# Optimization experiments

Measured on AMD Instinct MI355X. Metric: run time of the kernel, lower is better.

Reference implementation:

```python
import jax, jax.numpy as jnp
import numpy as np

N_NODES = 50000
NNZ = 800000
HYPER_DIM = 128
N_LAYERS = 2
LEAKY = 0.2
LN_EPS = 1e-5


def setup_inputs() -> dict:
    key = jax.random.key(0)
    k1, k2, k3, k4 = jax.random.split(key, 4)
    return {
        "ego_embeddings": jax.random.normal(k1, (N_NODES, HYPER_DIM), dtype=jnp.float32),
        "adj_vals": jax.random.uniform(k2, (NNZ,), dtype=jnp.float32),
        "ln_gamma": jnp.ones((N_LAYERS, HYPER_DIM), dtype=jnp.float32),
        "ln_beta": jnp.zeros((N_LAYERS, HYPER_DIM), dtype=jnp.float32),
        "adj_rows": jax.random.randint(k3, (NNZ,), 0, N_NODES, dtype=jnp.int32),
        "adj_cols": jax.random.randint(k4, (NNZ,), 0, N_NODES, dtype=jnp.int32),
        "n_users": 25000,
    }


def _spmm(rows, cols, vals, x, n_out):
    # y = A @ x for sparse A in COO (rows, cols, vals): gather + segment-sum
    return jax.ops.segment_sum(vals[:, None] * x[cols], rows, num_segments=n_out)


def _layer_norm(x, gamma, beta):
    mu = jnp.mean(x, axis=-1, keepdims=True)
    var = jnp.mean(jnp.square(x - mu), axis=-1, keepdims=True)
    return (x - mu) * jax.lax.rsqrt(var + LN_EPS) * gamma + beta


def reference(ego_embeddings, adj_vals, ln_gamma, ln_beta, adj_rows, adj_cols, n_users):
    res = ego_embeddings
    embs = ego_embeddings
    for k in range(N_LAYERS):
        # adj.T @ embs  (rows of A^T are cols of A)
        ht = _spmm(adj_cols, adj_rows, adj_vals, embs, N_NODES)
        # adj @ (adj.T @ embs)
        h = _spmm(adj_rows, adj_cols, adj_vals, ht, N_NODES)
        if k != N_LAYERS - 1:
            h = jnp.where(h >= 0, h, LEAKY * h)  # LeakyReLU
        embs = _layer_norm(h, ln_gamma[k], ln_beta[k]) + res
    user_emb = embs[:n_users]
    item_emb = embs[n_users:]
    return (user_emb, item_emb)
```

## Files before the change

kernel.cpp:

```cpp
#include <hip/hip_runtime.h>
#include <hip/hip_bf16.h>

#define HD 128
#define PB 256
#define LEAKY 0.2f
#define LN_EPS 1e-5f

__device__ __forceinline__ unsigned short bfr(float f) {
    unsigned int b = __float_as_uint(f);
    return (unsigned short)((b + 0x7fffu + ((b >> 16) & 1u)) >> 16);
}
__device__ __forceinline__ float blo(unsigned int u) { return __uint_as_float(u << 16); }
__device__ __forceinline__ float bhi(unsigned int u) { return __uint_as_float(u & 0xffff0000u); }

__global__ __launch_bounds__(256) void f32_to_bf16(
    const float* __restrict__ x, unsigned short* __restrict__ y, int n4) {
    int i = blockIdx.x * 256 + threadIdx.x;
    if (i >= n4) return;
    float4 f = ((const float4*)x)[i];
    ushort4 u;
    u.x = bfr(f.x); u.y = bfr(f.y); u.z = bfr(f.z); u.w = bfr(f.w);
    ((ushort4*)y)[i] = u;
}


__global__ __launch_bounds__(256) void part_count(
    const int* __restrict__ rows, const int* __restrict__ cols,
    int* __restrict__ counts, int nnz) {
    __shared__ int cR[64], cC[64];
    if (threadIdx.x < 64) { cR[threadIdx.x] = 0; cC[threadIdx.x] = 0; }
    __syncthreads();
    int chunk = (nnz + PB - 1) / PB;
    int beg = blockIdx.x * chunk;
    int end = min(beg + chunk, nnz);
    for (int i = beg + threadIdx.x; i < end; i += 256) {
        atomicAdd(&cR[rows[i] >> 10], 1);
        atomicAdd(&cC[cols[i] >> 10], 1);
    }
    __syncthreads();
    if (threadIdx.x < 64) {
        counts[(size_t)blockIdx.x * 64 + threadIdx.x] = cR[threadIdx.x];
        counts[(size_t)PB * 64 + blockIdx.x * 64 + threadIdx.x] = cC[threadIdx.x];
    }
}

__global__ __launch_bounds__(64) void part_off(
    int* __restrict__ counts, int* __restrict__ totals) {
    int bkt = blockIdx.x, dir = blockIdx.y, lane = threadIdx.x;
    int* p = counts + (size_t)dir * PB * 64;
    int v[4], s = 0;
    #pragma unroll
    for (int j = 0; j < 4; ++j) {
        int blk = lane * 4 + j;
        v[j] = p[(size_t)blk * 64 + bkt];
        s += v[j];
    }
    int incl = s;
    #pragma unroll
    for (int off = 1; off < 64; off <<= 1) {
        int t = __shfl_up(incl, off);
        if (lane >= off) incl += t;
    }
    int excl = incl - s;
    #pragma unroll
    for (int j = 0; j < 4; ++j) {
        int blk = lane * 4 + j;
        p[(size_t)blk * 64 + bkt] = excl;
        excl += v[j];
    }
    if (lane == 63) totals[dir * 64 + bkt] = incl;
}

__global__ __launch_bounds__(128) void base_scan(
    const int* __restrict__ totals, int* __restrict__ bases,
    int* __restrict__ rp_r, int* __restrict__ rp_c, int nbk, int n, int nnz) {
    int dir = threadIdx.x >> 6, lane = threadIdx.x & 63;
    int v = (lane < nbk) ? totals[dir * 64 + lane] : 0;
    int incl = v;
    #pragma unroll
    for (int off = 1; off < 64; off <<= 1) {
        int t = __shfl_up(incl, off);
        if (lane >= off) incl += t;
    }
    bases[dir * 64 + lane] = incl - v;
    if (lane == 0) (dir ? rp_c : rp_r)[n] = nnz;
}

__global__ __launch_bounds__(256) void part_scatter(
    const int* __restrict__ rows, const int* __restrict__ cols,
    const float* __restrict__ vals,
    const int* __restrict__ counts, const int* __restrict__ bases,
    uint2* __restrict__ stg_r, uint2* __restrict__ stg_c, int nnz) {
    __shared__ int cR[64], cC[64], wbR[64], wbC[64];
    if (threadIdx.x < 64) {
        cR[threadIdx.x] = 0; cC[threadIdx.x] = 0;
        wbR[threadIdx.x] = bases[threadIdx.x] +
            counts[(size_t)blockIdx.x * 64 + threadIdx.x];
        wbC[threadIdx.x] = bases[64 + threadIdx.x] +
            counts[(size_t)PB * 64 + blockIdx.x * 64 + threadIdx.x];
    }
    __syncthreads();
    int chunk = (nnz + PB - 1) / PB;
    int beg = blockIdx.x * chunk;
    int end = min(beg + chunk, nnz);
    for (int i = beg + threadIdx.x; i < end; i += 256) {
        int ro = rows[i], co = cols[i];
        unsigned vb = (unsigned)bfr(vals[i]) << 16;
        int rk = atomicAdd(&cR[ro >> 10], 1);
        stg_r[wbR[ro >> 10] + rk] = make_uint2(vb | (unsigned)co, (unsigned)ro);
        int ck = atomicAdd(&cC[co >> 10], 1);
        stg_c[wbC[co >> 10] + ck] = make_uint2(vb | (unsigned)ro, (unsigned)co);
    }
}

__global__ __launch_bounds__(1024) void bucket_build(
    const uint2* __restrict__ stg_r, const uint2* __restrict__ stg_c,
    const int* __restrict__ totals, const int* __restrict__ bases,
    unsigned* __restrict__ ent_r, unsigned* __restrict__ ent_c,
    int* __restrict__ rp_r, int* __restrict__ rp_c, int n) {
    __shared__ int cnt[1024];
    __shared__ int wsum[16], woff[16];
    int bkt = blockIdx.x, dir = blockIdx.y;
    const uint2* stg = dir ? stg_c : stg_r;
    unsigned* ent = dir ? ent_c : ent_r;
    int* rp = dir ? rp_c : rp_r;
    int base = bases[dir * 64 + bkt];
    int total = totals[dir * 64 + bkt];
    int lo = bkt << 10;
    int nb = min(1024, n - lo);
    cnt[threadIdx.x] = 0;
    __syncthreads();
    for (int i = threadIdx.x; i < total; i += 1024)
        atomicAdd(&cnt[(int)stg[base + i].y - lo], 1);
    __syncthreads();
    int lane = threadIdx.x & 63, wid = threadIdx.x >> 6;
    int v = cnt[threadIdx.x];
    int incl = v;
    #pragma unroll
    for (int off = 1; off < 64; off <<= 1) {
        int t = __shfl_up(incl, off);
        if (lane >= off) incl += t;
    }
    if (lane == 63) wsum[wid] = incl;
    __syncthreads();
    if (threadIdx.x == 0) {
        int run = 0;
        #pragma unroll
        for (int w = 0; w < 16; ++w) { woff[w] = run; run += wsum[w]; }
    }
    __syncthreads();
    int excl = woff[wid] + incl - v;
    if (threadIdx.x < nb) rp[lo + threadIdx.x] = base + excl;
    cnt[threadIdx.x] = excl;
    __syncthreads();
    for (int i = threadIdx.x; i < total; i += 1024) {
        uint2 e = stg[base + i];
        int pos = atomicAdd(&cnt[(int)e.y - lo], 1);
        ent[base + pos] = e.x;
    }
}

__global__ __launch_bounds__(256) void spmm_bf(
    const unsigned short* __restrict__ x, const int* __restrict__ rp,
    const unsigned* __restrict__ ent,
    const float* __restrict__ res, const float* __restrict__ gamma,
    const float* __restrict__ beta,
    unsigned short* __restrict__ out_bf, float* __restrict__ out_f32,
    int n, int post) {
    int wid = threadIdx.x >> 6, lane = threadIdx.x & 63;
    int row = blockIdx.x * 4 + wid;
    if (row >= n) return;
    int quarter = lane >> 4, q = lane & 15;
    int beg = rp[row], end = rp[row + 1];
    float acc[8];
    #pragma unroll
    for (int k = 0; k < 8; ++k) acc[k] = 0.f;

    int i = beg + quarter;
    for (; i + 12 < end; i += 16) {
        unsigned e0 = ent[i], e1 = ent[i + 4], e2 = ent[i + 8], e3 = ent[i + 12];
        uint4 u0 = ((const uint4*)(x + (size_t)(e0 & 0xffffu) * HD))[q];
        uint4 u1 = ((const uint4*)(x + (size_t)(e1 & 0xffffu) * HD))[q];
        uint4 u2 = ((const uint4*)(x + (size_t)(e2 & 0xffffu) * HD))[q];
        uint4 u3 = ((const uint4*)(x + (size_t)(e3 & 0xffffu) * HD))[q];
        float v0 = bhi(e0), v1 = bhi(e1), v2 = bhi(e2), v3 = bhi(e3);
        acc[0] += v0 * blo(u0.x) + v1 * blo(u1.x);
        acc[1] += v0 * bhi(u0.x) + v1 * bhi(u1.x);
        acc[2] += v0 * blo(u0.y) + v1 * blo(u1.y);
        acc[3] += v0 * bhi(u0.y) + v1 * bhi(u1.y);
        acc[4] += v0 * blo(u0.z) + v1 * blo(u1.z);
        acc[5] += v0 * bhi(u0.z) + v1 * bhi(u1.z);
        acc[6] += v0 * blo(u0.w) + v1 * blo(u1.w);
        acc[7] += v0 * bhi(u0.w) + v1 * bhi(u1.w);
        acc[0] += v2 * blo(u2.x) + v3 * blo(u3.x);
        acc[1] += v2 * bhi(u2.x) + v3 * bhi(u3.x);
        acc[2] += v2 * blo(u2.y) + v3 * blo(u3.y);
        acc[3] += v2 * bhi(u2.y) + v3 * bhi(u3.y);
        acc[4] += v2 * blo(u2.z) + v3 * blo(u3.z);
        acc[5] += v2 * bhi(u2.z) + v3 * bhi(u3.z);
        acc[6] += v2 * blo(u2.w) + v3 * blo(u3.w);
        acc[7] += v2 * bhi(u2.w) + v3 * bhi(u3.w);
    }
    for (; i < end; i += 4) {
        unsigned e0 = ent[i];
        uint4 u0 = ((const uint4*)(x + (size_t)(e0 & 0xffffu) * HD))[q];
        float v0 = bhi(e0);
        acc[0] += v0 * blo(u0.x);
        acc[1] += v0 * bhi(u0.x);
        acc[2] += v0 * blo(u0.y);
        acc[3] += v0 * bhi(u0.y);
        acc[4] += v0 * blo(u0.z);
        acc[5] += v0 * bhi(u0.z);
        acc[6] += v0 * blo(u0.w);
        acc[7] += v0 * bhi(u0.w);
    }
    #pragma unroll
    for (int k = 0; k < 8; ++k) {
        acc[k] += __shfl_xor(acc[k], 16);
        acc[k] += __shfl_xor(acc[k], 32);
    }
    if (quarter != 0) return;

    if (post == 0) {
        uint4 s;
        s.x = (unsigned)bfr(acc[0]) | ((unsigned)bfr(acc[1]) << 16);
        s.y = (unsigned)bfr(acc[2]) | ((unsigned)bfr(acc[3]) << 16);
        s.z = (unsigned)bfr(acc[4]) | ((unsigned)bfr(acc[5]) << 16);
        s.w = (unsigned)bfr(acc[6]) | ((unsigned)bfr(acc[7]) << 16);
        ((uint4*)(out_bf + (size_t)row * HD))[q] = s;
        return;
    }
    if (post == 1) {
        #pragma unroll
        for (int k = 0; k < 8; ++k) acc[k] = acc[k] >= 0.f ? acc[k] : LEAKY * acc[k];
    }
    float t = 0.f;
    #pragma unroll
    for (int k = 0; k < 8; ++k) t += acc[k];
    #pragma unroll
    for (int off = 1; off < 16; off <<= 1) t += __shfl_xor(t, off);
    float mu = t * (1.f / HD);
    float d[8], vs = 0.f;
    #pragma unroll
    for (int k = 0; k < 8; ++k) { d[k] = acc[k] - mu; vs += d[k] * d[k]; }
    #pragma unroll
    for (int off = 1; off < 16; off <<= 1) vs += __shfl_xor(vs, off);
    float inv = rsqrtf(vs * (1.f / HD) + LN_EPS);

    float4 g0 = ((const float4*)gamma)[2 * q], g1 = ((const float4*)gamma)[2 * q + 1];
    float4 b0 = ((const float4*)beta)[2 * q],  b1 = ((const float4*)beta)[2 * q + 1];
    float4 r0 = ((const float4*)(res + (size_t)row * HD))[2 * q];
    float4 r1 = ((const float4*)(res + (size_t)row * HD))[2 * q + 1];
    float o[8];
    o[0] = d[0] * inv * g0.x + b0.x + r0.x;
    o[1] = d[1] * inv * g0.y + b0.y + r0.y;
    o[2] = d[2] * inv * g0.z + b0.z + r0.z;
    o[3] = d[3] * inv * g0.w + b0.w + r0.w;
    o[4] = d[4] * inv * g1.x + b1.x + r1.x;
    o[5] = d[5] * inv * g1.y + b1.y + r1.y;
    o[6] = d[6] * inv * g1.z + b1.z + r1.z;
    o[7] = d[7] * inv * g1.w + b1.w + r1.w;
    if (post == 1) {
        uint4 s;
        s.x = (unsigned)bfr(o[0]) | ((unsigned)bfr(o[1]) << 16);
        s.y = (unsigned)bfr(o[2]) | ((unsigned)bfr(o[3]) << 16);
        s.z = (unsigned)bfr(o[4]) | ((unsigned)bfr(o[5]) << 16);
        s.w = (unsigned)bfr(o[6]) | ((unsigned)bfr(o[7]) << 16);
        ((uint4*)(out_bf + (size_t)row * HD))[q] = s;
    } else {
        float4 s0 = {o[0], o[1], o[2], o[3]};
        float4 s1 = {o[4], o[5], o[6], o[7]};
        ((float4*)(out_f32 + (size_t)row * HD))[2 * q] = s0;
        ((float4*)(out_f32 + (size_t)row * HD))[2 * q + 1] = s1;
    }
}

extern "C" void kernel_launch(void* const* d_in, const int* in_sizes, int n_in,
                              void* d_out, int out_size, void* d_ws, size_t ws_size,
                              hipStream_t stream) {
    const float* ego   = (const float*)d_in[0];
    const float* vals  = (const float*)d_in[1];
    const float* gamma = (const float*)d_in[2];
    const float* beta  = (const float*)d_in[3];
    const int*   rows  = (const int*)d_in[4];
    const int*   cols  = (const int*)d_in[5];

    const int N   = in_sizes[0] / HD;
    const int NNZ = in_sizes[1];
    const int NBK = (N + 1023) >> 10;

    float* out = (float*)d_out;
    char* w = (char*)d_ws;
    unsigned short* ego_bf = (unsigned short*)w; w += (size_t)N * HD * 2;
    unsigned short* bufA   = (unsigned short*)w; w += (size_t)N * HD * 2;
    unsigned short* bufB   = (unsigned short*)w; w += (size_t)N * HD * 2;
    int*  rp_r = (int*)w;  w += (size_t)(N + 4) * 4;
    int*  rp_c = (int*)w;  w += (size_t)(N + 4) * 4;
    unsigned* ent_r = (unsigned*)w; w += (size_t)NNZ * 4;
    unsigned* ent_c = (unsigned*)w; w += (size_t)NNZ * 4;
    int* counts = (int*)w; w += (size_t)2 * PB * 64 * 4;
    int* totals = (int*)w; w += 128 * 4;
    int* bases  = (int*)w; w += 128 * 4;

    uint2* stg_r = (uint2*)bufB;
    uint2* stg_c = stg_r + NNZ;

    f32_to_bf16<<<(N * HD / 4 + 255) / 256, 256, 0, stream>>>(ego, ego_bf, N * HD / 4);
    part_count<<<PB, 256, 0, stream>>>(rows, cols, counts, NNZ);
    part_off<<<dim3(NBK, 2), 64, 0, stream>>>(counts, totals);
    base_scan<<<1, 128, 0, stream>>>(totals, bases, rp_r, rp_c, NBK, N, NNZ);
    part_scatter<<<PB, 256, 0, stream>>>(rows, cols, vals, counts, bases,
                                         stg_r, stg_c, NNZ);
    bucket_build<<<dim3(NBK, 2), 1024, 0, stream>>>(stg_r, stg_c, totals, bases,
                                                    ent_r, ent_c, rp_r, rp_c, N);

    const int sblocks = (N + 3) / 4;

    spmm_bf<<<sblocks, 256, 0, stream>>>(ego_bf, rp_c, ent_c,
                                         nullptr, nullptr, nullptr, bufA, nullptr, N, 0);
    spmm_bf<<<sblocks, 256, 0, stream>>>(bufA, rp_r, ent_r,
                                         ego, gamma, beta, bufB, nullptr, N, 1);
    spmm_bf<<<sblocks, 256, 0, stream>>>(bufB, rp_c, ent_c,
                                         nullptr, nullptr, nullptr, bufA, nullptr, N, 0);
    spmm_bf<<<sblocks, 256, 0, stream>>>(bufA, rp_r, ent_r,
                                         ego, gamma + HD, beta + HD, nullptr, out, N, 2);
}
```

Baseline: 267.2 us.

## Fuse bf16 conversion and base scan into partition kernels, read residual as bf16

The standalone f32-to-bf16 conversion is folded into part_count as a grid-stride loop. The single-block base_scan kernel is removed: each part_scatter block and each bucket_build block now recomputes the bucket bases from totals itself, and bucket_build writes the rp[n] sentinel. The residual in the layer-norm epilogue is read from the bf16 copy instead of fp32, which halves that read. Together this drops two kernel launches and some residual traffic, at the cost of redundant scans per block and lower precision in the residual add.

Result: no change. 268.1 us (+0.3%).

```diff
diff --git a/kernel.cpp b/kernel.cpp
--- a/kernel.cpp
+++ b/kernel.cpp
@@ -13,20 +13,12 @@
 __device__ __forceinline__ float blo(unsigned int u) { return __uint_as_float(u << 16); }
 __device__ __forceinline__ float bhi(unsigned int u) { return __uint_as_float(u & 0xffff0000u); }
 
-__global__ __launch_bounds__(256) void f32_to_bf16(
-    const float* __restrict__ x, unsigned short* __restrict__ y, int n4) {
-    int i = blockIdx.x * 256 + threadIdx.x;
-    if (i >= n4) return;
-    float4 f = ((const float4*)x)[i];
-    ushort4 u;
-    u.x = bfr(f.x); u.y = bfr(f.y); u.z = bfr(f.z); u.w = bfr(f.w);
-    ((ushort4*)y)[i] = u;
-}
-
 
 __global__ __launch_bounds__(256) void part_count(
     const int* __restrict__ rows, const int* __restrict__ cols,
-    int* __restrict__ counts, int nnz) {
+    int* __restrict__ counts,
+    const float* __restrict__ ego, unsigned short* __restrict__ ego_bf,
+    int nnz, int n4) {
     __shared__ int cR[64], cC[64];
     if (threadIdx.x < 64) { cR[threadIdx.x] = 0; cC[threadIdx.x] = 0; }
     __syncthreads();
@@ -37,6 +29,12 @@
         atomicAdd(&cR[rows[i] >> 10], 1);
         atomicAdd(&cC[cols[i] >> 10], 1);
     }
+    for (int i = blockIdx.x * 256 + threadIdx.x; i < n4; i += 256 * PB) {
+        float4 f = ((const float4*)ego)[i];
+        ushort4 u;
+        u.x = bfr(f.x); u.y = bfr(f.y); u.z = bfr(f.z); u.w = bfr(f.w);
+        ((ushort4*)ego_bf)[i] = u;
+    }
     __syncthreads();
     if (threadIdx.x < 64) {
         counts[(size_t)blockIdx.x * 64 + threadIdx.x] = cR[threadIdx.x];
@@ -71,33 +69,25 @@
     if (lane == 63) totals[dir * 64 + bkt] = incl;
 }
 
-__global__ __launch_bounds__(128) void base_scan(
-    const int* __restrict__ totals, int* __restrict__ bases,
-    int* __restrict__ rp_r, int* __restrict__ rp_c, int nbk, int n, int nnz) {
-    int dir = threadIdx.x >> 6, lane = threadIdx.x & 63;
-    int v = (lane < nbk) ? totals[dir * 64 + lane] : 0;
-    int incl = v;
-    #pragma unroll
-    for (int off = 1; off < 64; off <<= 1) {
-        int t = __shfl_up(incl, off);
-        if (lane >= off) incl += t;
-    }
-    bases[dir * 64 + lane] = incl - v;
-    if (lane == 0) (dir ? rp_c : rp_r)[n] = nnz;
-}
-
 __global__ __launch_bounds__(256) void part_scatter(
     const int* __restrict__ rows, const int* __restrict__ cols,
     const float* __restrict__ vals,
-    const int* __restrict__ counts, const int* __restrict__ bases,
-    uint2* __restrict__ stg_r, uint2* __restrict__ stg_c, int nnz) {
+    const int* __restrict__ counts, const int* __restrict__ totals,
+    uint2* __restrict__ stg_r, uint2* __restrict__ stg_c, int nnz, int nbk) {
     __shared__ int cR[64], cC[64], wbR[64], wbC[64];
     if (threadIdx.x < 64) {
-        cR[threadIdx.x] = 0; cC[threadIdx.x] = 0;
-        wbR[threadIdx.x] = bases[threadIdx.x] +
-            counts[(size_t)blockIdx.x * 64 + threadIdx.x];
-        wbC[threadIdx.x] = bases[64 + threadIdx.x] +
-            counts[(size_t)PB * 64 + blockIdx.x * 64 + threadIdx.x];
+        int t = threadIdx.x;
+        cR[t] = 0; cC[t] = 0;
+        int vR = (t < nbk) ? totals[t] : 0;
+        int vC = (t < nbk) ? totals[64 + t] : 0;
+        int iR = vR, iC = vC;
+        #pragma unroll
+        for (int off = 1; off < 64; off <<= 1) {
+            int a = __shfl_up(iR, off), b = __shfl_up(iC, off);
+            if (t >= off) { iR += a; iC += b; }
+        }
+        wbR[t] = iR - vR + counts[(size_t)blockIdx.x * 64 + t];
+        wbC[t] = iC - vC + counts[(size_t)PB * 64 + blockIdx.x * 64 + t];
     }
     __syncthreads();
     int chunk = (nnz + PB - 1) / PB;
@@ -115,21 +105,28 @@
 
 __global__ __launch_bounds__(1024) void bucket_build(
     const uint2* __restrict__ stg_r, const uint2* __restrict__ stg_c,
-    const int* __restrict__ totals, const int* __restrict__ bases,
+    const int* __restrict__ totals,
     unsigned* __restrict__ ent_r, unsigned* __restrict__ ent_c,
-    int* __restrict__ rp_r, int* __restrict__ rp_c, int n) {
+    int* __restrict__ rp_r, int* __restrict__ rp_c, int n, int nnz) {
     __shared__ int cnt[1024];
     __shared__ int wsum[16], woff[16];
+    __shared__ int s_base;
     int bkt = blockIdx.x, dir = blockIdx.y;
     const uint2* stg = dir ? stg_c : stg_r;
     unsigned* ent = dir ? ent_c : ent_r;
     int* rp = dir ? rp_c : rp_r;
-    int base = bases[dir * 64 + bkt];
+    if (threadIdx.x < 64) {
+        int v = (threadIdx.x < bkt) ? totals[dir * 64 + threadIdx.x] : 0;
+        #pragma unroll
+        for (int off = 32; off; off >>= 1) v += __shfl_xor(v, off);
+        if (threadIdx.x == 0) s_base = v;
+    }
+    cnt[threadIdx.x] = 0;
+    __syncthreads();
+    int base = s_base;
     int total = totals[dir * 64 + bkt];
     int lo = bkt << 10;
     int nb = min(1024, n - lo);
-    cnt[threadIdx.x] = 0;
-    __syncthreads();
     for (int i = threadIdx.x; i < total; i += 1024)
         atomicAdd(&cnt[(int)stg[base + i].y - lo], 1);
     __syncthreads();
@@ -151,6 +148,7 @@
     __syncthreads();
     int excl = woff[wid] + incl - v;
     if (threadIdx.x < nb) rp[lo + threadIdx.x] = base + excl;
+    if (bkt == gridDim.x - 1 && threadIdx.x == 0) rp[n] = nnz;
     cnt[threadIdx.x] = excl;
     __syncthreads();
     for (int i = threadIdx.x; i < total; i += 1024) {
@@ -163,7 +161,7 @@
 __global__ __launch_bounds__(256) void spmm_bf(
     const unsigned short* __restrict__ x, const int* __restrict__ rp,
     const unsigned* __restrict__ ent,
-    const float* __restrict__ res, const float* __restrict__ gamma,
+    const unsigned short* __restrict__ res, const float* __restrict__ gamma,
     const float* __restrict__ beta,
     unsigned short* __restrict__ out_bf, float* __restrict__ out_f32,
     int n, int post) {
@@ -249,17 +247,16 @@
 
     float4 g0 = ((const float4*)gamma)[2 * q], g1 = ((const float4*)gamma)[2 * q + 1];
     float4 b0 = ((const float4*)beta)[2 * q],  b1 = ((const float4*)beta)[2 * q + 1];
-    float4 r0 = ((const float4*)(res + (size_t)row * HD))[2 * q];
-    float4 r1 = ((const float4*)(res + (size_t)row * HD))[2 * q + 1];
+    uint4 ru = ((const uint4*)(res + (size_t)row * HD))[q];
     float o[8];
-    o[0] = d[0] * inv * g0.x + b0.x + r0.x;
-    o[1] = d[1] * inv * g0.y + b0.y + r0.y;
-    o[2] = d[2] * inv * g0.z + b0.z + r0.z;
-    o[3] = d[3] * inv * g0.w + b0.w + r0.w;
-    o[4] = d[4] * inv * g1.x + b1.x + r1.x;
-    o[5] = d[5] * inv * g1.y + b1.y + r1.y;
-    o[6] = d[6] * inv * g1.z + b1.z + r1.z;
-    o[7] = d[7] * inv * g1.w + b1.w + r1.w;
+    o[0] = d[0] * inv * g0.x + b0.x + blo(ru.x);
+    o[1] = d[1] * inv * g0.y + b0.y + bhi(ru.x);
+    o[2] = d[2] * inv * g0.z + b0.z + blo(ru.y);
+    o[3] = d[3] * inv * g0.w + b0.w + bhi(ru.y);
+    o[4] = d[4] * inv * g1.x + b1.x + blo(ru.z);
+    o[5] = d[5] * inv * g1.y + b1.y + bhi(ru.z);
+    o[6] = d[6] * inv * g1.z + b1.z + blo(ru.w);
+    o[7] = d[7] * inv * g1.w + b1.w + bhi(ru.w);
     if (post == 1) {
         uint4 s;
         s.x = (unsigned)bfr(o[0]) | ((unsigned)bfr(o[1]) << 16);
@@ -300,28 +297,27 @@
     unsigned* ent_c = (unsigned*)w; w += (size_t)NNZ * 4;
     int* counts = (int*)w; w += (size_t)2 * PB * 64 * 4;
     int* totals = (int*)w; w += 128 * 4;
-    int* bases  = (int*)w; w += 128 * 4;
 
     uint2* stg_r = (uint2*)bufB;
     uint2* stg_c = stg_r + NNZ;
 
-    f32_to_bf16<<<(N * HD / 4 + 255) / 256, 256, 0, stream>>>(ego, ego_bf, N * HD / 4);
-    part_count<<<PB, 256, 0, stream>>>(rows, cols, counts, NNZ);
+    part_count<<<PB, 256, 0, stream>>>(rows, cols, counts, ego, ego_bf,
+                                       NNZ, N * HD / 4);
     part_off<<<dim3(NBK, 2), 64, 0, stream>>>(counts, totals);
-    base_scan<<<1, 128, 0, stream>>>(totals, bases, rp_r, rp_c, NBK, N, NNZ);
-    part_scatter<<<PB, 256, 0, stream>>>(rows, cols, vals, counts, bases,
-                                         stg_r, stg_c, NNZ);
-    bucket_build<<<dim3(NBK, 2), 1024, 0, stream>>>(stg_r, stg_c, totals, bases,
-                                                    ent_r, ent_c, rp_r, rp_c, N);
+    part_scatter<<<PB, 256, 0, stream>>>(rows, cols, vals, counts, totals,
+                                         stg_r, stg_c, NNZ, NBK);
+    bucket_build<<<dim3(NBK, 2), 1024, 0, stream>>>(stg_r, stg_c, totals,
+                                                    ent_r, ent_c, rp_r, rp_c,
+                                                    N, NNZ);
 
     const int sblocks = (N + 3) / 4;
 
     spmm_bf<<<sblocks, 256, 0, stream>>>(ego_bf, rp_c, ent_c,
                                          nullptr, nullptr, nullptr, bufA, nullptr, N, 0);
     spmm_bf<<<sblocks, 256, 0, stream>>>(bufA, rp_r, ent_r,
-                                         ego, gamma, beta, bufB, nullptr, N, 1);
+                                         ego_bf, gamma, beta, bufB, nullptr, N, 1);
     spmm_bf<<<sblocks, 256, 0, stream>>>(bufB, rp_c, ent_c,
                                          nullptr, nullptr, nullptr, bufA, nullptr, N, 0);
     spmm_bf<<<sblocks, 256, 0, stream>>>(bufA, rp_r, ent_r,
-                                         ego, gamma + HD, beta + HD, nullptr, out, N, 2);
-}
+                                         ego_bf, gamma + HD, beta + HD, nullptr, out, N, 2);
+}
```
